# Kernel tuning notes

Measured on AMD Instinct MI355X. Metric: run time of the kernel, lower is better.

## Reference

```python
import jax, jax.numpy as jnp
import numpy as np

# Dims: B=4, C_in=256, H=W=64 -> L=4096, token_dim D=256, state_dim N=512, K=4
B_, C_IN, H_, W_ = 4, 256, 64, 64
D, N, K = 256, 512, 4


def setup_inputs() -> dict:
    key = jax.random.key(0)
    ks = jax.random.split(key, 16)
    g = lambda k, shape, sc=0.02: (jax.random.normal(k, shape, jnp.float32) * sc)
    return {
        'feat_map': jax.random.normal(ks[0], (B_, C_IN, H_, W_), jnp.float32),
        'hf_map':   jax.random.normal(ks[1], (B_, C_IN, H_, W_), jnp.float32),
        # 1x1 conv proj_f / proj_hf: weight (out=D, in=C_IN), bias (D,)
        'Wf':  g(ks[2], (D, C_IN)), 'bf':  jnp.zeros((D,), jnp.float32),
        'Whf': g(ks[3], (D, C_IN)), 'bhf': jnp.zeros((D,), jnp.float32),
        # alpha_head: Linear(D, D//2) -> GELU -> Linear(D//2, K)
        'Wa1': g(ks[4], (D // 2, D)), 'ba1': jnp.zeros((D // 2,), jnp.float32),
        'Wa2': g(ks[5], (K, D // 2)), 'ba2': jnp.zeros((K,), jnp.float32),
        # SelectiveSSM base tuples: diagonal decay logits A (K,N), input maps B (K,N,D), output maps C (K,D,N)
        'A_base': g(ks[6], (K, N), 1.0),
        'B_base': g(ks[7], (K, N, D), 0.02),
        'C_base': g(ks[8], (K, D, N), 0.02),
        # out_proj 1x1 conv: (C_IN, D)
        'Wout': g(ks[9], (C_IN, D)), 'bout': jnp.zeros((C_IN,), jnp.float32),
    }


def _stage(feat_map, hf_map, Wf, bf, Whf, bhf, Wa1, ba1, Wa2, ba2,
           A_base, B_base, C_base, Wout, bout):
    B, C, H, W = feat_map.shape
    L = H * W
    # 1x1 conv token projections -> (B, L, D)
    t_f = jnp.einsum('bchw,dc->bdhw', feat_map, Wf) + bf[None, :, None, None]
    t_hf = jnp.einsum('bchw,dc->bdhw', hf_map, Whf) + bhf[None, :, None, None]
    x = t_f.reshape(B, -1, L).transpose(0, 2, 1)        # (B, L, D)
    t_hf_seq = t_hf.reshape(B, -1, L).transpose(0, 2, 1)  # (B, L, D)
    # gating MLP -> per-token mixture weights over K base SSMs
    hmid = jax.nn.gelu(t_hf_seq @ Wa1.T + ba1, approximate=False)
    alpha = jax.nn.softmax(hmid @ Wa2.T + ba2, axis=-1)  # (B, L, K)
    # selective SSM: per-token mixed diagonal decay and input drive
    a = jax.nn.sigmoid(jnp.einsum('blk,kn->bln', alpha, A_base))   # (B, L, N)
    u = jnp.einsum('bld,blk,knd->bln', x, alpha, B_base)           # (B, L, N)

    def step(h, au):
        a_t, u_t = au                   # each (B, N)
        h = a_t * h + u_t
        return h, h

    h0 = jnp.zeros((B, a.shape[-1]), x.dtype)
    _, hs = jax.lax.scan(step, h0, (a.transpose(1, 0, 2), u.transpose(1, 0, 2)))
    h_seq = hs.transpose(1, 0, 2)                                   # (B, L, N)
    # mixed readout
    y = jnp.einsum('blk,bln,kdn->bld', alpha, h_seq, C_base)        # (B, L, D)
    y_map = y.transpose(0, 2, 1).reshape(B, -1, H, W)
    out = jnp.einsum('bdhw,cd->bchw', y_map, Wout) + bout[None, :, None, None]
    return out


def reference(feat_map, hf_map, Wf, bf, Whf, bhf, Wa1, ba1, Wa2, ba2,
              A_base, B_base, C_base, Wout, bout):
    return _stage(feat_map, hf_map, Wf, bf, Whf, bhf, Wa1, ba1, Wa2, ba2,
                  A_base, B_base, C_base, Wout, bout)
```

## Files before the change

kernel.cpp:

```cpp
#include <hip/hip_runtime.h>
#include <hip/hip_bf16.h>
#include <math.h>

#define B_  4
#define CIN 256
#define L_  4096
#define D_  256
#define N_  512
#define K_  4
#define DH  128
#define BL  (B_ * L_)

#define NCHUNK 128
#define CLEN   (L_ / NCHUNK)

typedef __attribute__((ext_vector_type(8))) short bfrag;
typedef __attribute__((ext_vector_type(4))) float f4;

__device__ __forceinline__ float bf2f(unsigned short u) {
  return __uint_as_float(((unsigned int)u) << 16);
}
__device__ __forceinline__ unsigned short f2bf(float f) {
  unsigned int u = __float_as_uint(f);
  return (unsigned short)((u + 0x7FFFu + ((u >> 16) & 1u)) >> 16);
}

__global__ void k_prep(const float* __restrict__ Wf, const float* __restrict__ Whf,
                       const float* __restrict__ Wa1, const float* __restrict__ Wout,
                       const float* __restrict__ Bb, const float* __restrict__ Cb,
                       const float* __restrict__ bfv, const float* __restrict__ bhfv,
                       unsigned short* __restrict__ Wfb ,
                       unsigned short* __restrict__ Wa1b,
                       unsigned short* __restrict__ Woutb,
                       unsigned short* __restrict__ Bb16,
                       unsigned short* __restrict__ Cb16,
                       float* __restrict__ biascat) {
  int i = blockIdx.x * 256 + threadIdx.x;
  if (i < 65536) { Wfb[i] = f2bf(Wf[i]); return; } i -= 65536;
  if (i < 65536) { Wfb[65536 + i] = f2bf(Whf[i]); return; } i -= 65536;
  if (i < 32768) { Wa1b[i] = f2bf(Wa1[i]); return; } i -= 32768;
  if (i < 65536) { Woutb[i] = f2bf(Wout[i]); return; } i -= 65536;
  if (i < 524288) {
    int d = i & 255, n = (i >> 8) & 511, k = i >> 17;
    Bb16[(((size_t)n << 2) | k) << 8 | d] = f2bf(Bb[i]);
    return;
  } i -= 524288;
  if (i < 524288) {
    int nn = i & 511, d = (i >> 9) & 255, k = i >> 17;
    Cb16[(((size_t)d << 2) | k) << 9 | nn] = f2bf(Cb[i]);
    return;
  } i -= 524288;
  if (i < 256) { biascat[i] = bfv[i]; return; } i -= 256;
  if (i < 256) { biascat[256 + i] = bhfv[i]; }
}

__global__ void k_transpose2(const float* __restrict__ feat, const float* __restrict__ hf,
                             unsigned short* __restrict__ featT ) {
  __shared__ float tile[32][33];
  const int z = blockIdx.z;
  const int b = z & 3, which = z >> 2;
  const float* in = which ? hf : feat;
  unsigned short* outT = featT + (size_t)which * BL * CIN;
  const int l0 = blockIdx.x * 32, c0 = blockIdx.y * 32;
  const int tx = threadIdx.x, ty = threadIdx.y;
  const float* p = in + ((size_t)b * CIN + c0 + ty) * L_ + l0 + tx;
#pragma unroll
  for (int i = 0; i < 32; i += 8) tile[ty + i][tx] = p[(size_t)i * L_];
  __syncthreads();
  unsigned short* q = outT + ((size_t)b * L_ + l0 + ty) * CIN + c0 + tx;
#pragma unroll
  for (int i = 0; i < 32; i += 8) q[(size_t)i * CIN] = f2bf(tile[tx][ty + i]);
}

__global__ void k_alpha(const float* __restrict__ hm0, const float* __restrict__ hm1,
                        const float* __restrict__ ba1, const float* __restrict__ Wa2,
                        const float* __restrict__ ba2, float* __restrict__ alpha) {
  __shared__ float w2[K_ * DH];
  __shared__ float b1[DH];
  __shared__ float b2[K_];
  for (int i = threadIdx.x; i < K_ * DH; i += 256) w2[i] = Wa2[i];
  if (threadIdx.x < DH) b1[threadIdx.x] = ba1[threadIdx.x];
  if (threadIdx.x < K_) b2[threadIdx.x] = ba2[threadIdx.x];
  __syncthreads();
  const int token = blockIdx.x * 64 + (threadIdx.x >> 2);
  const int q = threadIdx.x & 3;
  float a0 = 0.f, a1 = 0.f, a2 = 0.f, a3 = 0.f;
  const size_t base = (size_t)token * DH + q * 32;
#pragma unroll
  for (int j4 = 0; j4 < 8; ++j4) {
    float4 h0 = *(const float4*)(hm0 + base + j4 * 4);
    float4 h1 = *(const float4*)(hm1 + base + j4 * 4);
    const float hv[4] = {h0.x + h1.x, h0.y + h1.y, h0.z + h1.z, h0.w + h1.w};
#pragma unroll
    for (int e = 0; e < 4; ++e) {
      const int d = q * 32 + j4 * 4 + e;
      float g = hv[e] + b1[d];
      g = 0.5f * g * (1.0f + erff(g * 0.70710678118654752f));
      a0 += g * w2[0 * DH + d];
      a1 += g * w2[1 * DH + d];
      a2 += g * w2[2 * DH + d];
      a3 += g * w2[3 * DH + d];
    }
  }
  a0 += __shfl_xor(a0, 1); a1 += __shfl_xor(a1, 1); a2 += __shfl_xor(a2, 1); a3 += __shfl_xor(a3, 1);
  a0 += __shfl_xor(a0, 2); a1 += __shfl_xor(a1, 2); a2 += __shfl_xor(a2, 2); a3 += __shfl_xor(a3, 2);
  a0 += b2[0]; a1 += b2[1]; a2 += b2[2]; a3 += b2[3];
  float m = fmaxf(fmaxf(a0, a1), fmaxf(a2, a3));
  float e0 = expf(a0 - m), e1 = expf(a1 - m), e2 = expf(a2 - m), e3 = expf(a3 - m);
  float inv = 1.f / (e0 + e1 + e2 + e3);
  float my = (q == 0) ? e0 : (q == 1) ? e1 : (q == 2) ? e2 : e3;
  alpha[(size_t)token * 4 + q] = my * inv;
}


__global__ void k_scanA(const unsigned short* __restrict__ u, const float* __restrict__ alpha,
                        const float* __restrict__ Abase,
                        float* __restrict__ P, float* __restrict__ Hend) {
  const int n = threadIdx.x;
  const int bc = blockIdx.x;
  const int b = bc >> 7, c = bc & 127;
  const float A0 = Abase[n], A1 = Abase[N_ + n], A2 = Abase[2 * N_ + n], A3 = Abase[3 * N_ + n];
  const size_t tok0 = (size_t)b * L_ + (size_t)c * CLEN;
  float p = 1.f, h = 0.f;
  for (int l = 0; l < CLEN; ++l) {
    const size_t t = tok0 + l;
    float4 al = *(const float4*)(alpha + t * 4);
    float s = al.x * A0 + al.y * A1 + al.z * A2 + al.w * A3;
    float av = 1.f / (1.f + expf(-s));
    float uv = bf2f(u[t * N_ + n]);
    h = av * h + uv;
    p *= av;
  }
  P[(size_t)bc * N_ + n] = p;
  Hend[(size_t)bc * N_ + n] = h;
}

__global__ void k_scanB(const float* __restrict__ P, const float* __restrict__ Hend,
                        float* __restrict__ Hstart) {
  const int n = threadIdx.x;
  const int b = blockIdx.x;
  float h = 0.f;
  for (int c = 0; c < NCHUNK; ++c) {
    size_t idx = ((size_t)b * NCHUNK + c) * N_ + n;
    Hstart[idx] = h;
    h = P[idx] * h + Hend[idx];
  }
}

__global__ void k_scanC(const unsigned short* __restrict__ u, const float* __restrict__ alpha,
                        const float* __restrict__ Abase, const float* __restrict__ Hstart,
                        unsigned short* __restrict__ hbf) {
  const int n = threadIdx.x;
  const int bc = blockIdx.x;
  const int b = bc >> 7, c = bc & 127;
  const float A0 = Abase[n], A1 = Abase[N_ + n], A2 = Abase[2 * N_ + n], A3 = Abase[3 * N_ + n];
  const size_t tok0 = (size_t)b * L_ + (size_t)c * CLEN;
  float h = Hstart[(size_t)bc * N_ + n];
  for (int l = 0; l < CLEN; ++l) {
    const size_t t = tok0 + l;
    float4 al = *(const float4*)(alpha + t * 4);
    float s = al.x * A0 + al.y * A1 + al.z * A2 + al.w * A3;
    float av = 1.f / (1.f + expf(-s));
    float uv = bf2f(u[t * N_ + n]);
    h = av * h + uv;
    hbf[t * N_ + n] = f2bf(h);
  }
}

#define BM 128
#define BN 128
#define BK 32

#define GLL(src, dst)                                                                      \
  __builtin_amdgcn_global_load_lds((const __attribute__((address_space(1))) void*)(src),   \
                                   (__attribute__((address_space(3))) void*)(dst), 16, 0, 0)

#define BM2 128
#define BN2 256

template <int BIAS, int EPI>
__global__ __launch_bounds__(512, 2) void gemm_bt2(
    const unsigned short* __restrict__ A, long sA,
    const unsigned short* __restrict__ Bm, long sB,
    const float* __restrict__ bias, long bS,
    const float* __restrict__ alphaP,
    void* __restrict__ Cv, long sC,
    int M, int N, int Kd, int lda, int ldb) {
  const int zb = blockIdx.z;
  A += (size_t)zb * sA;
  Bm += (size_t)zb * sB;
  if (BIAS) bias += (size_t)zb * bS;
  const int m0 = blockIdx.x * BM2;
  const int n0 = blockIdx.y * BN2;
  __shared__ __attribute__((aligned(16))) unsigned short As[3 * BM2 * BK];
  __shared__ __attribute__((aligned(16))) unsigned short Bs[3 * BN2 * BK];
  const int t = threadIdx.x;
  const int lane = t & 63;
  const int w = t >> 6;
  const int wm = (w >> 2) * 64;
  const int wn = (w & 3) * 64;

  f4 acc[4][4];
#pragma unroll
  for (int i = 0; i < 4; ++i)
#pragma unroll
    for (int j = 0; j < 4; ++j) acc[i][j] = (f4){0.f, 0.f, 0.f, 0.f};

  const int rS = t >> 2;
  const int cS = (((t & 3) ^ ((t >> 3) & 3))) * 8;
  const unsigned short* gA = A + (size_t)(m0 + rS) * lda + cS;
  const unsigned short* gB = Bm + (size_t)(n0 + rS) * ldb + cS;
  const long rowStepB = (long)128 * ldb;
  const int r16 = lane & 15;
  const int sx = (r16 >> 1) & 3;
  const int kg = (((lane >> 4) ^ sx)) * 8;

#define STAGE2(slot, kt)                                                \
  do {                                                                  \
    const unsigned short* sA_ = gA + (size_t)(kt) * BK;                 \
    const unsigned short* sB_ = gB + (size_t)(kt) * BK;                 \
    unsigned short* dA_ = As + (slot) * (BM2 * BK) + t * 8;             \
    unsigned short* dB_ = Bs + (slot) * (BN2 * BK) + t * 8;             \
    GLL(sA_, dA_);                                                      \
    GLL(sB_, dB_);                                                      \
    GLL(sB_ + rowStepB, dB_ + BM2 * BK);                                \
  } while (0)

  const int nIter = Kd / BK;
  STAGE2(0, 0);
  STAGE2(1, 1);
  int slot = 0;
  for (int kt = 0; kt < nIter; ++kt) {
    if (kt + 1 < nIter) asm volatile("s_waitcnt vmcnt(3)" ::: "memory");
    else                asm volatile("s_waitcnt vmcnt(0)" ::: "memory");
    __builtin_amdgcn_s_barrier();
    asm volatile("" ::: "memory");
    if (kt + 2 < nIter) {
      int s2 = slot + 2; if (s2 >= 3) s2 -= 3;
      STAGE2(s2, kt + 2);
    }
    const unsigned short* Ab = As + slot * (BM2 * BK);
    const unsigned short* Bb2 = Bs + slot * (BN2 * BK);
    bfrag af[4], bfr[4];
#pragma unroll
    for (int i = 0; i < 4; ++i) {
      af[i]  = *(const bfrag*)(Ab + (wm + i * 16 + r16) * BK + kg);
      bfr[i] = *(const bfrag*)(Bb2 + (wn + i * 16 + r16) * BK + kg);
    }
    __builtin_amdgcn_s_setprio(1);
#pragma unroll
    for (int i = 0; i < 4; ++i)
#pragma unroll
      for (int j = 0; j < 4; ++j)
        acc[i][j] = __builtin_amdgcn_mfma_f32_16x16x32_bf16(af[i], bfr[j], acc[i][j], 0, 0, 0);
    __builtin_amdgcn_s_setprio(0);
    asm volatile("" ::: "memory");
    slot = (slot == 2) ? 0 : slot + 1;
  }
#undef STAGE2

  const int rowBase = m0 + wm + ((lane >> 4) << 2);
  const int colBase = n0 + wn + (lane & 15);

  if (EPI >= 2) {
    const int kq = lane & 3;
    const int NO = N >> 2;
    float av[4][4];
#pragma unroll
    for (int i = 0; i < 4; ++i)
#pragma unroll
      for (int r = 0; r < 4; ++r)
        av[i][r] = alphaP[(size_t)(rowBase + i * 16 + r) * 4 + kq];
    float* Cf = (float*)Cv + (size_t)zb * sC;
    unsigned short* Cb = (unsigned short*)Cv + (size_t)zb * sC;
#pragma unroll
    for (int i = 0; i < 4; ++i)
#pragma unroll
      for (int j = 0; j < 4; ++j) {
        const int col = colBase + j * 16;
#pragma unroll
        for (int r = 0; r < 4; ++r) {
          float p = av[i][r] * acc[i][j][r];
          p += __shfl_xor(p, 1);
          p += __shfl_xor(p, 2);
          if (kq == 0) {
            const int row = rowBase + i * 16 + r;
            if (EPI == 2) Cf[(size_t)row * NO + (col >> 2)] = p;
            else          Cb[(size_t)row * NO + (col >> 2)] = f2bf(p);
          }
        }
      }
    return;
  }

  float* Cf = (float*)Cv + (size_t)zb * sC;
  unsigned short* Cb = (unsigned short*)Cv + (size_t)zb * sC;
#pragma unroll
  for (int i = 0; i < 4; ++i) {
#pragma unroll
    for (int j = 0; j < 4; ++j) {
      const int col = colBase + j * 16;
#pragma unroll
      for (int r = 0; r < 4; ++r) {
        const int row = rowBase + i * 16 + r;
        float v = acc[i][j][r];
        if (BIAS == 1) v += bias[col];
        if (BIAS == 2) v += bias[row];
        if (EPI == 1) Cb[(size_t)row * N + col] = f2bf(v);
        else          Cf[(size_t)row * N + col] = v;
      }
    }
  }
}

template <int BIAS, int EPI >
__global__ __launch_bounds__(256) void gemm_bt3(
    const unsigned short* __restrict__ A, long sA,
    const unsigned short* __restrict__ Bm, long sB,
    const float* __restrict__ bias, long bS,
    void* __restrict__ Cv, long sC,
    int M, int N, int Kd, int lda, int ldb) {
  const int zb = blockIdx.z;
  A += (size_t)zb * sA;
  Bm += (size_t)zb * sB;
  if (BIAS) bias += (size_t)zb * bS;
  const int m0 = blockIdx.x * BM;
  const int n0 = blockIdx.y * BN;
  __shared__ __attribute__((aligned(16))) unsigned short As[3 * BM * BK];
  __shared__ __attribute__((aligned(16))) unsigned short Bs[3 * BN * BK];
  const int t = threadIdx.x;
  const int lane = t & 63;
  const int w = t >> 6;
  const int wm = (w >> 1) * 64;
  const int wn = (w & 1) * 64;

  f4 acc[4][4];
#pragma unroll
  for (int i = 0; i < 4; ++i)
#pragma unroll
    for (int j = 0; j < 4; ++j) acc[i][j] = (f4){0.f, 0.f, 0.f, 0.f};

  const int rS = t >> 2;
  const int cS = (((t & 3) ^ ((t >> 3) & 3))) * 8;
  const unsigned short* gA = A + (size_t)(m0 + rS) * lda + cS;
  const unsigned short* gB = Bm + (size_t)(n0 + rS) * ldb + cS;
  const long rowStepA = (long)64 * lda;
  const long rowStepB = (long)64 * ldb;
  const int r16 = lane & 15;
  const int sx = (r16 >> 1) & 3;
  const int kg = (((lane >> 4) ^ sx)) * 8;

#define STAGE3(slot, kt)                                                \
  do {                                                                  \
    const unsigned short* sA_ = gA + (size_t)(kt) * BK;                 \
    const unsigned short* sB_ = gB + (size_t)(kt) * BK;                 \
    unsigned short* dA_ = As + (slot) * (BM * BK) + t * 8;              \
    unsigned short* dB_ = Bs + (slot) * (BN * BK) + t * 8;              \
    GLL(sA_, dA_); GLL(sA_ + rowStepA, dA_ + 64 * BK);                  \
    GLL(sB_, dB_); GLL(sB_ + rowStepB, dB_ + 64 * BK);                  \
  } while (0)

  const int nIter = Kd / BK;
  STAGE3(0, 0);
  STAGE3(1, 1);
  int slot = 0;
  for (int kt = 0; kt < nIter; ++kt) {
    if (kt + 1 < nIter) asm volatile("s_waitcnt vmcnt(4)" ::: "memory");
    else                asm volatile("s_waitcnt vmcnt(0)" ::: "memory");
    __builtin_amdgcn_s_barrier();
    asm volatile("" ::: "memory");
    if (kt + 2 < nIter) {
      int s2 = slot + 2; if (s2 >= 3) s2 -= 3;
      STAGE3(s2, kt + 2);
    }
    const unsigned short* Ab = As + slot * (BM * BK);
    const unsigned short* Bb2 = Bs + slot * (BN * BK);
    bfrag af[4], bfr[4];
#pragma unroll
    for (int i = 0; i < 4; ++i) {
      af[i]  = *(const bfrag*)(Ab + (wm + i * 16 + r16) * BK + kg);
      bfr[i] = *(const bfrag*)(Bb2 + (wn + i * 16 + r16) * BK + kg);
    }
    __builtin_amdgcn_s_setprio(1);
#pragma unroll
    for (int i = 0; i < 4; ++i)
#pragma unroll
      for (int j = 0; j < 4; ++j)
        acc[i][j] = __builtin_amdgcn_mfma_f32_16x16x32_bf16(af[i], bfr[j], acc[i][j], 0, 0, 0);
    __builtin_amdgcn_s_setprio(0);
    asm volatile("" ::: "memory");
    slot = (slot == 2) ? 0 : slot + 1;
  }
#undef STAGE3

  const int rowBase = m0 + wm + ((lane >> 4) << 2);
  const int colBase = n0 + wn + (lane & 15);
  float* Cf = (float*)Cv + (size_t)zb * sC;
  unsigned short* Cb = (unsigned short*)Cv + (size_t)zb * sC;
#pragma unroll
  for (int i = 0; i < 4; ++i) {
#pragma unroll
    for (int j = 0; j < 4; ++j) {
      const int col = colBase + j * 16;
#pragma unroll
      for (int r = 0; r < 4; ++r) {
        const int row = rowBase + i * 16 + r;
        float v = acc[i][j][r];
        if (BIAS == 1) v += bias[col];
        if (BIAS == 2) v += bias[row];
        if (EPI == 1) Cb[(size_t)row * N + col] = f2bf(v);
        else          Cf[(size_t)row * N + col] = v;
      }
    }
  }
}


extern "C" void kernel_launch(void* const* d_in, const int* in_sizes, int n_in,
                              void* d_out, int out_size, void* d_ws, size_t ws_size,
                              hipStream_t stream) {
  const float* feat  = (const float*)d_in[0];
  const float* hf    = (const float*)d_in[1];
  const float* Wf    = (const float*)d_in[2];
  const float* bfv   = (const float*)d_in[3];
  const float* Whf   = (const float*)d_in[4];
  const float* bhfv  = (const float*)d_in[5];
  const float* Wa1   = (const float*)d_in[6];
  const float* ba1   = (const float*)d_in[7];
  const float* Wa2   = (const float*)d_in[8];
  const float* ba2   = (const float*)d_in[9];
  const float* Abase = (const float*)d_in[10];
  const float* Bbase = (const float*)d_in[11];
  const float* Cbase = (const float*)d_in[12];
  const float* Wout  = (const float*)d_in[13];
  const float* bout  = (const float*)d_in[14];
  float* out = (float*)d_out;

  char* ws = (char*)d_ws;
  size_t off = 0;
  auto alloc = [&](size_t bytes) { void* p = ws + off; off += bytes; return p; };

  unsigned short* Wfb    = (unsigned short*)alloc((size_t)2 * D_ * CIN * 2);
  unsigned short* Wa1b   = (unsigned short*)alloc((size_t)DH * D_ * 2);
  unsigned short* Woutb  = (unsigned short*)alloc((size_t)CIN * D_ * 2);
  unsigned short* Bb16   = (unsigned short*)alloc((size_t)K_ * N_ * D_ * 2);
  unsigned short* Cb16   = (unsigned short*)alloc((size_t)K_ * D_ * N_ * 2);
  float*          biascat= (float*)alloc((size_t)2 * D_ * 4);
  float*          alpha  = (float*)alloc((size_t)BL * K_ * 4);
  float*          Pc     = (float*)alloc((size_t)B_ * NCHUNK * N_ * 4);
  float*          He     = (float*)alloc((size_t)B_ * NCHUNK * N_ * 4);
  float*          Hs     = (float*)alloc((size_t)B_ * NCHUNK * N_ * 4);
  unsigned short* hbf    = (unsigned short*)alloc((size_t)BL * N_ * 2);
  unsigned short* x      = (unsigned short*)alloc((size_t)BL * D_ * 2);
  unsigned short* thf    = (unsigned short*)alloc((size_t)BL * D_ * 2);
  unsigned short* featT  = (unsigned short*)alloc((size_t)BL * CIN * 2);
  unsigned short* hfT    = (unsigned short*)alloc((size_t)BL * CIN * 2);
  unsigned short* u16    = (unsigned short*)alloc((size_t)BL * N_ * 2);

  float*          hm0 = (float*)featT;
  float*          hm1 = (float*)hfT;
  unsigned short* y   = thf;

  if (ws_size < off) return;

  k_prep<<<dim3((3 * 65536 + 32768 + 2 * 524288 + 512 + 255) / 256), 256, 0, stream>>>(
      Wf, Whf, Wa1, Wout, Bbase, Cbase, bfv, bhfv, Wfb, Wa1b, Woutb, Bb16, Cb16, biascat);

  k_transpose2<<<dim3(L_ / 32, CIN / 32, 2 * B_), dim3(32, 8), 0, stream>>>(feat, hf, featT);

  gemm_bt2<1, 1><<<dim3(BL / BM2, D_ / BN2, 2), 512, 0, stream>>>(
      featT, (long)BL * CIN, Wfb, (long)D_ * CIN, biascat, D_, nullptr,
      x, (long)BL * D_, BL, D_, CIN, CIN, CIN);

  gemm_bt3<0, 0><<<dim3(BL / BM, DH / BN, 2), 256, 0, stream>>>(
      thf, 128, Wa1b, 128, nullptr, 0,
      hm0, (long)BL * DH, BL, DH, 128, D_, D_);
  k_alpha<<<dim3(BL / 64), 256, 0, stream>>>(hm0, hm1, ba1, Wa2, ba2, alpha);

  gemm_bt2<0, 3><<<dim3(BL / BM2, (K_ * N_) / BN2, 1), 512, 0, stream>>>(
      x, 0, Bb16, 0, nullptr, 0, alpha, u16, 0, BL, K_ * N_, D_, D_, D_);

  k_scanA<<<dim3(B_ * NCHUNK), N_, 0, stream>>>(u16, alpha, Abase, Pc, He);
  k_scanB<<<dim3(B_), N_, 0, stream>>>(Pc, He, Hs);
  k_scanC<<<dim3(B_ * NCHUNK), N_, 0, stream>>>(u16, alpha, Abase, Hs, hbf);

  gemm_bt2<0, 3><<<dim3(BL / BM2, (K_ * D_) / BN2, 1), 512, 0, stream>>>(
      hbf, 0, Cb16, 0, nullptr, 0, alpha, y, 0, BL, K_ * D_, N_, N_, N_);

  gemm_bt3<2, 0><<<dim3(CIN / BM, L_ / BN, B_), 256, 0, stream>>>(
      Woutb, 0, y, (long)L_ * D_, bout, 0, out, (long)CIN * L_, CIN, L_, D_, D_, D_);
}
```

Before: 160.4 us.

## Add 256x256 GEMM kernel with alpha-mixing epilogue for SSM input/readout projections

Introduces gemm8p, a 256x256x64 tile bf16 MFMA GEMM with XOR-swizzled LDS, double buffering, and staged prefetch interleaved between MFMA phases. It keeps the alpha-weighted K-reduction epilogue and replaces gemm_bt2<0,3> for both the u projection and the C readout. The alpha epilogue is removed from gemm_bt2. Larger tiles raise data reuse per block, but they also raise register pressure and halve the block count, which may hurt occupancy and wave balance.

```diff
diff --git a/kernel.cpp b/kernel.cpp
--- a/kernel.cpp
+++ b/kernel.cpp
@@ -175,6 +175,179 @@
   __builtin_amdgcn_global_load_lds((const __attribute__((address_space(1))) void*)(src),   \
                                    (__attribute__((address_space(3))) void*)(dst), 16, 0, 0)
 
+#define BM4 256
+#define BN4 256
+#define BK4 64
+
+__global__ __launch_bounds__(512, 2) void gemm8p(
+    const unsigned short* __restrict__ A,
+    const unsigned short* __restrict__ Bm,
+    const float* __restrict__ alphaP,
+    unsigned short* __restrict__ C,
+    int N, int Kd) {
+  const int m0 = blockIdx.x * BM4;
+  const int n0 = blockIdx.y * BN4;
+  __shared__ __attribute__((aligned(16))) unsigned short As[2][BM4 * BK4];
+  __shared__ __attribute__((aligned(16))) unsigned short Bs[2][BN4 * BK4];
+  const int t = threadIdx.x;
+  const int lane = t & 63;
+  const int w = t >> 6;
+  const int wm = (w >> 2) * 128;
+  const int wn = (w & 3) * 64;
+  const int r16 = lane & 15;
+  const int g = lane >> 4;
+  const int srow = t >> 3;
+  const int sslot = (t & 7) ^ (srow & 7);
+  const int kof0 = ((g ^ (r16 & 7))) * 8;
+  const int kof1 = (((4 + g) ^ (r16 & 7))) * 8;
+
+  f4 acc[8][4];
+#pragma unroll
+  for (int i = 0; i < 8; ++i)
+#pragma unroll
+    for (int j = 0; j < 4; ++j) acc[i][j] = (f4){0.f, 0.f, 0.f, 0.f};
+
+#define STG4(dst, src, rowbase, kt2, half)                                             \
+  do {                                                                                 \
+    const unsigned short* s_ = (src) + (size_t)((rowbase) + (half) * 128 + srow) * Kd  \
+                               + (size_t)(kt2) * BK4 + sslot * 8;                      \
+    unsigned short* d_ = (dst) + (half) * 128 * BK4 + t * 8;                           \
+    GLL(s_, d_);                                                                       \
+    GLL(s_ + (size_t)64 * Kd, d_ + 64 * BK4);                                          \
+  } while (0)
+
+  const int nkt = Kd / BK4;
+  STG4(As[0], A, m0, 0, 0);  STG4(As[0], A, m0, 0, 1);
+  STG4(Bs[0], Bm, n0, 0, 0); STG4(Bs[0], Bm, n0, 0, 1);
+  asm volatile("s_waitcnt vmcnt(0)" ::: "memory");
+  __builtin_amdgcn_s_barrier();
+  asm volatile("" ::: "memory");
+
+  int buf = 0;
+  for (int kt = 0; kt < nkt; ++kt) {
+    const unsigned short* Ab = As[buf];
+    const unsigned short* Bb = Bs[buf];
+    const int nb = buf ^ 1;
+    const bool pre = (kt + 1 < nkt);
+    bfrag bfr[4][2];
+    bfrag af[2][2];
+
+#pragma unroll
+    for (int fc = 0; fc < 4; ++fc) {
+      bfr[fc][0] = *(const bfrag*)(Bb + (wn + fc * 16 + r16) * BK4 + kof0);
+      bfr[fc][1] = *(const bfrag*)(Bb + (wn + fc * 16 + r16) * BK4 + kof1);
+    }
+#pragma unroll
+    for (int f = 0; f < 2; ++f) {
+      af[f][0] = *(const bfrag*)(Ab + (wm + (0 + f) * 16 + r16) * BK4 + kof0);
+      af[f][1] = *(const bfrag*)(Ab + (wm + (0 + f) * 16 + r16) * BK4 + kof1);
+    }
+    if (pre) { STG4(As[nb], A, m0, kt + 1, 0); STG4(As[nb], A, m0, kt + 1, 1); }
+    __builtin_amdgcn_s_barrier();
+    asm volatile("s_waitcnt lgkmcnt(0)" ::: "memory");
+    __builtin_amdgcn_s_setprio(1);
+#pragma unroll
+    for (int f = 0; f < 2; ++f)
+#pragma unroll
+      for (int fc = 0; fc < 4; ++fc) {
+        acc[0 + f][fc] = __builtin_amdgcn_mfma_f32_16x16x32_bf16(af[f][0], bfr[fc][0], acc[0 + f][fc], 0, 0, 0);
+        acc[0 + f][fc] = __builtin_amdgcn_mfma_f32_16x16x32_bf16(af[f][1], bfr[fc][1], acc[0 + f][fc], 0, 0, 0);
+      }
+    __builtin_amdgcn_s_setprio(0);
+    asm volatile("" ::: "memory");
+    __builtin_amdgcn_s_barrier();
+    asm volatile("" ::: "memory");
+
+#pragma unroll
+    for (int f = 0; f < 2; ++f) {
+      af[f][0] = *(const bfrag*)(Ab + (wm + (2 + f) * 16 + r16) * BK4 + kof0);
+      af[f][1] = *(const bfrag*)(Ab + (wm + (2 + f) * 16 + r16) * BK4 + kof1);
+    }
+    if (pre) { STG4(Bs[nb], Bm, n0, kt + 1, 0); STG4(Bs[nb], Bm, n0, kt + 1, 1); }
+    __builtin_amdgcn_s_barrier();
+    asm volatile("s_waitcnt lgkmcnt(0)" ::: "memory");
+    __builtin_amdgcn_s_setprio(1);
+#pragma unroll
+    for (int f = 0; f < 2; ++f)
+#pragma unroll
+      for (int fc = 0; fc < 4; ++fc) {
+        acc[2 + f][fc] = __builtin_amdgcn_mfma_f32_16x16x32_bf16(af[f][0], bfr[fc][0], acc[2 + f][fc], 0, 0, 0);
+        acc[2 + f][fc] = __builtin_amdgcn_mfma_f32_16x16x32_bf16(af[f][1], bfr[fc][1], acc[2 + f][fc], 0, 0, 0);
+      }
+    __builtin_amdgcn_s_setprio(0);
+    asm volatile("" ::: "memory");
+    __builtin_amdgcn_s_barrier();
+    asm volatile("" ::: "memory");
+
+#pragma unroll
+    for (int f = 0; f < 2; ++f) {
+      af[f][0] = *(const bfrag*)(Ab + (wm + (4 + f) * 16 + r16) * BK4 + kof0);
+      af[f][1] = *(const bfrag*)(Ab + (wm + (4 + f) * 16 + r16) * BK4 + kof1);
+    }
+    __builtin_amdgcn_s_barrier();
+    asm volatile("s_waitcnt lgkmcnt(0)" ::: "memory");
+    __builtin_amdgcn_s_setprio(1);
+#pragma unroll
+    for (int f = 0; f < 2; ++f)
+#pragma unroll
+      for (int fc = 0; fc < 4; ++fc) {
+        acc[4 + f][fc] = __builtin_amdgcn_mfma_f32_16x16x32_bf16(af[f][0], bfr[fc][0], acc[4 + f][fc], 0, 0, 0);
+        acc[4 + f][fc] = __builtin_amdgcn_mfma_f32_16x16x32_bf16(af[f][1], bfr[fc][1], acc[4 + f][fc], 0, 0, 0);
+      }
+    __builtin_amdgcn_s_setprio(0);
+    asm volatile("" ::: "memory");
+    __builtin_amdgcn_s_barrier();
+    asm volatile("" ::: "memory");
+
+#pragma unroll
+    for (int f = 0; f < 2; ++f) {
+      af[f][0] = *(const bfrag*)(Ab + (wm + (6 + f) * 16 + r16) * BK4 + kof0);
+      af[f][1] = *(const bfrag*)(Ab + (wm + (6 + f) * 16 + r16) * BK4 + kof1);
+    }
+    __builtin_amdgcn_s_barrier();
+    asm volatile("s_waitcnt lgkmcnt(0)" ::: "memory");
+    __builtin_amdgcn_s_setprio(1);
+#pragma unroll
+    for (int f = 0; f < 2; ++f)
+#pragma unroll
+      for (int fc = 0; fc < 4; ++fc) {
+        acc[6 + f][fc] = __builtin_amdgcn_mfma_f32_16x16x32_bf16(af[f][0], bfr[fc][0], acc[6 + f][fc], 0, 0, 0);
+        acc[6 + f][fc] = __builtin_amdgcn_mfma_f32_16x16x32_bf16(af[f][1], bfr[fc][1], acc[6 + f][fc], 0, 0, 0);
+      }
+    __builtin_amdgcn_s_setprio(0);
+    asm volatile("s_waitcnt vmcnt(0)" ::: "memory");
+    __builtin_amdgcn_s_barrier();
+    asm volatile("" ::: "memory");
+
+    buf ^= 1;
+  }
+#undef STG4
+
+  const int rowBase = m0 + wm + (g << 2);
+  const int colBase = n0 + wn + r16;
+  const int kq = lane & 3;
+  const int NO = N >> 2;
+  float av[8][4];
+#pragma unroll
+  for (int i = 0; i < 8; ++i)
+#pragma unroll
+    for (int r = 0; r < 4; ++r)
+      av[i][r] = alphaP[(size_t)(rowBase + i * 16 + r) * 4 + kq];
+#pragma unroll
+  for (int i = 0; i < 8; ++i)
+#pragma unroll
+    for (int j = 0; j < 4; ++j) {
+      const int col = colBase + j * 16;
+#pragma unroll
+      for (int r = 0; r < 4; ++r) {
+        float p = av[i][r] * acc[i][j][r];
+        p += __shfl_xor(p, 1);
+        p += __shfl_xor(p, 2);
+        if (kq == 0) C[(size_t)(rowBase + i * 16 + r) * NO + (col >> 2)] = f2bf(p);
+      }
+    }
+}
+
 #define BM2 128
 #define BN2 256
 
@@ -183,7 +356,6 @@
     const unsigned short* __restrict__ A, long sA,
     const unsigned short* __restrict__ Bm, long sB,
     const float* __restrict__ bias, long bS,
-    const float* __restrict__ alphaP,
     void* __restrict__ Cv, long sC,
     int M, int N, int Kd, int lda, int ldb) {
   const int zb = blockIdx.z;
@@ -261,38 +433,6 @@
 
   const int rowBase = m0 + wm + ((lane >> 4) << 2);
   const int colBase = n0 + wn + (lane & 15);
-
-  if (EPI >= 2) {
-    const int kq = lane & 3;
-    const int NO = N >> 2;
-    float av[4][4];
-#pragma unroll
-    for (int i = 0; i < 4; ++i)
-#pragma unroll
-      for (int r = 0; r < 4; ++r)
-        av[i][r] = alphaP[(size_t)(rowBase + i * 16 + r) * 4 + kq];
-    float* Cf = (float*)Cv + (size_t)zb * sC;
-    unsigned short* Cb = (unsigned short*)Cv + (size_t)zb * sC;
-#pragma unroll
-    for (int i = 0; i < 4; ++i)
-#pragma unroll
-      for (int j = 0; j < 4; ++j) {
-        const int col = colBase + j * 16;
-#pragma unroll
-        for (int r = 0; r < 4; ++r) {
-          float p = av[i][r] * acc[i][j][r];
-          p += __shfl_xor(p, 1);
-          p += __shfl_xor(p, 2);
-          if (kq == 0) {
-            const int row = rowBase + i * 16 + r;
-            if (EPI == 2) Cf[(size_t)row * NO + (col >> 2)] = p;
-            else          Cb[(size_t)row * NO + (col >> 2)] = f2bf(p);
-          }
-        }
-      }
-    return;
-  }
-
   float* Cf = (float*)Cv + (size_t)zb * sC;
   unsigned short* Cb = (unsigned short*)Cv + (size_t)zb * sC;
 #pragma unroll
@@ -469,7 +609,7 @@
   k_transpose2<<<dim3(L_ / 32, CIN / 32, 2 * B_), dim3(32, 8), 0, stream>>>(feat, hf, featT);
 
   gemm_bt2<1, 1><<<dim3(BL / BM2, D_ / BN2, 2), 512, 0, stream>>>(
-      featT, (long)BL * CIN, Wfb, (long)D_ * CIN, biascat, D_, nullptr,
+      featT, (long)BL * CIN, Wfb, (long)D_ * CIN, biascat, D_,
       x, (long)BL * D_, BL, D_, CIN, CIN, CIN);
 
   gemm_bt3<0, 0><<<dim3(BL / BM, DH / BN, 2), 256, 0, stream>>>(
@@ -477,15 +617,15 @@
       hm0, (long)BL * DH, BL, DH, 128, D_, D_);
   k_alpha<<<dim3(BL / 64), 256, 0, stream>>>(hm0, hm1, ba1, Wa2, ba2, alpha);
 
-  gemm_bt2<0, 3><<<dim3(BL / BM2, (K_ * N_) / BN2, 1), 512, 0, stream>>>(
-      x, 0, Bb16, 0, nullptr, 0, alpha, u16, 0, BL, K_ * N_, D_, D_, D_);
+  gemm8p<<<dim3(BL / BM4, (K_ * N_) / BN4), 512, 0, stream>>>(
+      x, Bb16, alpha, u16, K_ * N_, D_);
 
   k_scanA<<<dim3(B_ * NCHUNK), N_, 0, stream>>>(u16, alpha, Abase, Pc, He);
   k_scanB<<<dim3(B_), N_, 0, stream>>>(Pc, He, Hs);
   k_scanC<<<dim3(B_ * NCHUNK), N_, 0, stream>>>(u16, alpha, Abase, Hs, hbf);
 
-  gemm_bt2<0, 3><<<dim3(BL / BM2, (K_ * D_) / BN2, 1), 512, 0, stream>>>(
-      hbf, 0, Cb16, 0, nullptr, 0, alpha, y, 0, BL, K_ * D_, N_, N_, N_);
+  gemm8p<<<dim3(BL / BM4, (K_ * D_) / BN4), 512, 0, stream>>>(
+      hbf, Cb16, alpha, y, K_ * D_, N_);
 
   gemm_bt3<2, 0><<<dim3(CIN / BM, L_ / BN, B_), 256, 0, stream>>>(
       Woutb, 0, y, (long)L_ * D_, bout, 0, out, (long)CIN * L_, CIN, L_, D_, D_, D_);
```

Result: slower. 171.8 us (+7.1%).

## Switch small GEMMs to 8-wave 128x128 kernel and store alpha-head hidden in bf16

Applied to the files above, without the earlier changes.

Replaces the 4-wave gemm_bt3 with an 8-wave variant: each wave computes a 64x32 sub-tile, each thread issues one global-to-LDS load per operand per stage, and launch bounds request two blocks per CU. The projection GEMM that used gemm_bt2 now uses this kernel too. The alpha-head hidden GEMM writes bf16 instead of fp32, and k_alpha reads packed bf16 pairs, halving that intermediate traffic. The aim is more waves in flight to hide latency on these short-K GEMMs, at the cost of less MFMA work per LDS fragment load and slightly lower precision in the gating path.

```diff
diff --git a/kernel.cpp b/kernel.cpp
--- a/kernel.cpp
+++ b/kernel.cpp
@@ -72,7 +72,8 @@
   for (int i = 0; i < 32; i += 8) q[(size_t)i * CIN] = f2bf(tile[tx][ty + i]);
 }
 
-__global__ void k_alpha(const float* __restrict__ hm0, const float* __restrict__ hm1,
+__global__ void k_alpha(const unsigned short* __restrict__ hm0,
+                        const unsigned short* __restrict__ hm1,
                         const float* __restrict__ ba1, const float* __restrict__ Wa2,
                         const float* __restrict__ ba2, float* __restrict__ alpha) {
   __shared__ float w2[K_ * DH];
@@ -87,19 +88,26 @@
   float a0 = 0.f, a1 = 0.f, a2 = 0.f, a3 = 0.f;
   const size_t base = (size_t)token * DH + q * 32;
 #pragma unroll
-  for (int j4 = 0; j4 < 8; ++j4) {
-    float4 h0 = *(const float4*)(hm0 + base + j4 * 4);
-    float4 h1 = *(const float4*)(hm1 + base + j4 * 4);
-    const float hv[4] = {h0.x + h1.x, h0.y + h1.y, h0.z + h1.z, h0.w + h1.w};
-#pragma unroll
-    for (int e = 0; e < 4; ++e) {
-      const int d = q * 32 + j4 * 4 + e;
-      float g = hv[e] + b1[d];
-      g = 0.5f * g * (1.0f + erff(g * 0.70710678118654752f));
-      a0 += g * w2[0 * DH + d];
-      a1 += g * w2[1 * DH + d];
-      a2 += g * w2[2 * DH + d];
-      a3 += g * w2[3 * DH + d];
+  for (int j8 = 0; j8 < 4; ++j8) {
+    uint4 v0 = *(const uint4*)(hm0 + base + j8 * 8);
+    uint4 v1 = *(const uint4*)(hm1 + base + j8 * 8);
+    const unsigned int* pa = (const unsigned int*)&v0;
+    const unsigned int* pb = (const unsigned int*)&v1;
+#pragma unroll
+    for (int p = 0; p < 4; ++p) {
+      float h0 = bf2f((unsigned short)(pa[p] & 0xffffu)) +
+                 bf2f((unsigned short)(pb[p] & 0xffffu));
+      float h1 = bf2f((unsigned short)(pa[p] >> 16)) +
+                 bf2f((unsigned short)(pb[p] >> 16));
+      const int d = q * 32 + j8 * 8 + p * 2;
+      float g0 = h0 + b1[d];
+      float g1 = h1 + b1[d + 1];
+      g0 = 0.5f * g0 * (1.0f + erff(g0 * 0.70710678118654752f));
+      g1 = 0.5f * g1 * (1.0f + erff(g1 * 0.70710678118654752f));
+      a0 += g0 * w2[0 * DH + d] + g1 * w2[0 * DH + d + 1];
+      a1 += g0 * w2[1 * DH + d] + g1 * w2[1 * DH + d + 1];
+      a2 += g0 * w2[2 * DH + d] + g1 * w2[2 * DH + d + 1];
+      a3 += g0 * w2[3 * DH + d] + g1 * w2[3 * DH + d + 1];
     }
   }
   a0 += __shfl_xor(a0, 1); a1 += __shfl_xor(a1, 1); a2 += __shfl_xor(a2, 1); a3 += __shfl_xor(a3, 1);
@@ -314,7 +322,7 @@
 }
 
 template <int BIAS, int EPI >
-__global__ __launch_bounds__(256) void gemm_bt3(
+__global__ __launch_bounds__(512, 2) void gemm_w8(
     const unsigned short* __restrict__ A, long sA,
     const unsigned short* __restrict__ Bm, long sB,
     const float* __restrict__ bias, long bS,
@@ -331,67 +339,62 @@
   const int t = threadIdx.x;
   const int lane = t & 63;
   const int w = t >> 6;
-  const int wm = (w >> 1) * 64;
-  const int wn = (w & 1) * 64;
-
-  f4 acc[4][4];
+  const int wm = (w >> 2) * 64;
+  const int wn = (w & 3) * 32;
+
+  f4 acc[4][2];
 #pragma unroll
   for (int i = 0; i < 4; ++i)
 #pragma unroll
-    for (int j = 0; j < 4; ++j) acc[i][j] = (f4){0.f, 0.f, 0.f, 0.f};
+    for (int j = 0; j < 2; ++j) acc[i][j] = (f4){0.f, 0.f, 0.f, 0.f};
 
   const int rS = t >> 2;
   const int cS = (((t & 3) ^ ((t >> 3) & 3))) * 8;
   const unsigned short* gA = A + (size_t)(m0 + rS) * lda + cS;
   const unsigned short* gB = Bm + (size_t)(n0 + rS) * ldb + cS;
-  const long rowStepA = (long)64 * lda;
-  const long rowStepB = (long)64 * ldb;
   const int r16 = lane & 15;
   const int sx = (r16 >> 1) & 3;
   const int kg = (((lane >> 4) ^ sx)) * 8;
 
-#define STAGE3(slot, kt)                                                \
+#define STAGEW(slot, kt)                                                \
   do {                                                                  \
-    const unsigned short* sA_ = gA + (size_t)(kt) * BK;                 \
-    const unsigned short* sB_ = gB + (size_t)(kt) * BK;                 \
-    unsigned short* dA_ = As + (slot) * (BM * BK) + t * 8;              \
-    unsigned short* dB_ = Bs + (slot) * (BN * BK) + t * 8;              \
-    GLL(sA_, dA_); GLL(sA_ + rowStepA, dA_ + 64 * BK);                  \
-    GLL(sB_, dB_); GLL(sB_ + rowStepB, dB_ + 64 * BK);                  \
+    GLL(gA + (size_t)(kt) * BK, As + (slot) * (BM * BK) + t * 8);       \
+    GLL(gB + (size_t)(kt) * BK, Bs + (slot) * (BN * BK) + t * 8);       \
   } while (0)
 
   const int nIter = Kd / BK;
-  STAGE3(0, 0);
-  STAGE3(1, 1);
+  STAGEW(0, 0);
+  STAGEW(1, 1);
   int slot = 0;
   for (int kt = 0; kt < nIter; ++kt) {
-    if (kt + 1 < nIter) asm volatile("s_waitcnt vmcnt(4)" ::: "memory");
+    if (kt + 1 < nIter) asm volatile("s_waitcnt vmcnt(2)" ::: "memory");
     else                asm volatile("s_waitcnt vmcnt(0)" ::: "memory");
     __builtin_amdgcn_s_barrier();
     asm volatile("" ::: "memory");
     if (kt + 2 < nIter) {
       int s2 = slot + 2; if (s2 >= 3) s2 -= 3;
-      STAGE3(s2, kt + 2);
+      STAGEW(s2, kt + 2);
     }
     const unsigned short* Ab = As + slot * (BM * BK);
     const unsigned short* Bb2 = Bs + slot * (BN * BK);
-    bfrag af[4], bfr[4];
-#pragma unroll
-    for (int i = 0; i < 4; ++i) {
+    bfrag af[4], bfr[2];
+#pragma unroll
+    for (int i = 0; i < 4; ++i)
       af[i]  = *(const bfrag*)(Ab + (wm + i * 16 + r16) * BK + kg);
-      bfr[i] = *(const bfrag*)(Bb2 + (wn + i * 16 + r16) * BK + kg);
-    }
+#pragma unroll
+    for (int j = 0; j < 2; ++j)
+      bfr[j] = *(const bfrag*)(Bb2 + (wn + j * 16 + r16) * BK + kg);
     __builtin_amdgcn_s_setprio(1);
 #pragma unroll
     for (int i = 0; i < 4; ++i)
 #pragma unroll
-      for (int j = 0; j < 4; ++j)
+      for (int j = 0; j < 2; ++j)
         acc[i][j] = __builtin_amdgcn_mfma_f32_16x16x32_bf16(af[i], bfr[j], acc[i][j], 0, 0, 0);
     __builtin_amdgcn_s_setprio(0);
     asm volatile("" ::: "memory");
     slot = (slot == 2) ? 0 : slot + 1;
   }
-#undef STAGE3
+#undef STAGEW
 
   const int rowBase = m0 + wm + ((lane >> 4) << 2);
   const int colBase = n0 + wn + (lane & 15);
@@ -400,7 +403,7 @@
 #pragma unroll
   for (int i = 0; i < 4; ++i) {
 #pragma unroll
-    for (int j = 0; j < 4; ++j) {
+    for (int j = 0; j < 2; ++j) {
       const int col = colBase + j * 16;
 #pragma unroll
       for (int r = 0; r < 4; ++r) {
@@ -457,8 +460,8 @@
   unsigned short* hfT    = (unsigned short*)alloc((size_t)BL * CIN * 2);
   unsigned short* u16    = (unsigned short*)alloc((size_t)BL * N_ * 2);
 
-  float*          hm0 = (float*)featT;
-  float*          hm1 = (float*)hfT;
+  unsigned short* hm0 = featT;
+  unsigned short* hm1 = featT + (size_t)BL * DH;
   unsigned short* y   = thf;
 
   if (ws_size < off) return;
@@ -468,11 +471,11 @@
 
   k_transpose2<<<dim3(L_ / 32, CIN / 32, 2 * B_), dim3(32, 8), 0, stream>>>(feat, hf, featT);
 
-  gemm_bt2<1, 1><<<dim3(BL / BM2, D_ / BN2, 2), 512, 0, stream>>>(
-      featT, (long)BL * CIN, Wfb, (long)D_ * CIN, biascat, D_, nullptr,
+  gemm_w8<1, 1><<<dim3(BL / BM, D_ / BN, 2), 512, 0, stream>>>(
+      featT, (long)BL * CIN, Wfb, (long)D_ * CIN, biascat, D_,
       x, (long)BL * D_, BL, D_, CIN, CIN, CIN);
 
-  gemm_bt3<0, 0><<<dim3(BL / BM, DH / BN, 2), 256, 0, stream>>>(
+  gemm_w8<0, 1><<<dim3(BL / BM, DH / BN, 2), 512, 0, stream>>>(
       thf, 128, Wa1b, 128, nullptr, 0,
       hm0, (long)BL * DH, BL, DH, 128, D_, D_);
   k_alpha<<<dim3(BL / 64), 256, 0, stream>>>(hm0, hm1, ba1, Wa2, ba2, alpha);
@@ -487,6 +490,6 @@
   gemm_bt2<0, 3><<<dim3(BL / BM2, (K_ * D_) / BN2, 1), 512, 0, stream>>>(
       hbf, 0, Cb16, 0, nullptr, 0, alpha, y, 0, BL, K_ * D_, N_, N_, N_);
 
-  gemm_bt3<2, 0><<<dim3(CIN / BM, L_ / BN, B_), 256, 0, stream>>>(
+  gemm_w8<2, 0><<<dim3(CIN / BM, L_ / BN, B_), 512, 0, stream>>>(
       Woutb, 0, y, (long)L_ * D_, bout, 0, out, (long)CIN * L_, CIN, L_, D_, D_, D_);
 }
```

Measured after the change: 156.0 us. 2.7% less time.
